# Performance work log

Measured on AMD Instinct MI355X. Metric: run time of the kernel, lower is better.

Reference implementation:

```python
import jax, jax.numpy as jnp
import numpy as np

N_NODES = 100000
N_FEAT = 512
HIDDEN = 64
N_CLASSES = 40
N_EDGES = 3200000
K = 10
ALPHA = 0.1


def setup_inputs() -> dict:
    key = jax.random.key(0)
    k1, k2, k3, k4 = jax.random.split(key, 4)
    x = jax.random.normal(k1, (N_NODES, N_FEAT), dtype=jnp.float32)
    # Glorot-ish scaled linear weights
    W1 = jax.random.normal(k2, (N_FEAT, HIDDEN), dtype=jnp.float32) / np.sqrt(N_FEAT)
    b1 = jnp.zeros((HIDDEN,), dtype=jnp.float32)
    W2 = jax.random.normal(k3, (HIDDEN, N_CLASSES), dtype=jnp.float32) / np.sqrt(HIDDEN)
    b2 = jnp.zeros((N_CLASSES,), dtype=jnp.float32)
    edge_index = jax.random.randint(k4, (2, N_EDGES), 0, N_NODES, dtype=jnp.int64)
    return {"x": x, "W1": W1, "b1": b1, "W2": W2, "b2": b2, "edge_index": edge_index}


def reference(x, W1, b1, W2, b2, edge_index):
    n = x.shape[0]
    # MLP (dropout is identity in eval mode)
    h = jnp.maximum(x @ W1 + b1, 0.0)
    h = h @ W2 + b2  # [N, C]

    # gcn_norm with self-loops: A_hat = D^{-1/2} (A + I) D^{-1/2}
    loops = jnp.arange(n, dtype=edge_index.dtype)
    row = jnp.concatenate([edge_index[0], loops])  # source (gather)
    col = jnp.concatenate([edge_index[1], loops])  # target (scatter)
    deg = jax.ops.segment_sum(jnp.ones(row.shape, dtype=h.dtype), col, num_segments=n)
    dinv = jnp.where(deg > 0, jax.lax.rsqrt(deg), 0.0)
    norm = dinv[row] * dinv[col]  # [E + N]

    h0 = h

    def step(z, _):
        msg = norm[:, None] * z[row]                      # gather + scale
        agg = jax.ops.segment_sum(msg, col, num_segments=n)  # scatter-add
        z = ALPHA * h0 + (1.0 - ALPHA) * agg
        return z, None

    z, _ = jax.lax.scan(step, h0, None, length=K)
    return jax.nn.log_softmax(z, axis=1)
```

## Files before the change

kernel.cpp:

```cpp
#include <hip/hip_runtime.h>
#include <hip/hip_bf16.h>
#include <hip/hip_fp16.h>

#define N_NODES   100000
#define N_FEAT    512
#define HIDDEN    64
#define N_CLASSES 40
#define KITER     10
#define ALPHA     0.1f
#define ZP        64
#define HPITCH    72
#define NXCD      8
#define WIN       (N_NODES / NXCD)
#define SUBCAP    65536
#define PARTB     2048
#define CAP       96

typedef __attribute__((ext_vector_type(8))) short bf16x8;
typedef __attribute__((ext_vector_type(4))) float f32x4;

__device__ __forceinline__ float bf2f(unsigned short u) {
    union { unsigned int i; float f; } c;
    c.i = ((unsigned int)u) << 16;
    return c.f;
}
__device__ __forceinline__ unsigned short f2bf(float f) {
    union { float f; unsigned int u; } c; c.f = f;
    unsigned int r = c.u + 0x7FFFu + ((c.u >> 16) & 1u);
    return (unsigned short)(r >> 16);
}

__global__ void zero_cur_kernel(int* __restrict__ cur, int* __restrict__ flags) {
    int t = threadIdx.x;
    if (t < 65) cur[t] = 0;
    if (t >= 65 && t < 67) flags[t - 65] = 0;
}

__global__ void detect_float_kernel(const unsigned short* __restrict__ w1raw,
                                    int* __restrict__ flags) {
    int i = blockIdx.x * blockDim.x + threadIdx.x;
    if (i < 32768) {
        unsigned short u = w1raw[i];
        if ((u & 0x7F80u) == 0x7F80u) atomicAdd(&flags[0], 1);
    }
}

__global__ void detect_edge_kernel(const int* __restrict__ ei, int* __restrict__ flags) {
    int i = blockIdx.x * blockDim.x + threadIdx.x;
    if (i < 2048) {
        if (ei[2 * i + 1] != 0) atomicAdd(&flags[1], 1);
    }
}

__global__ void pack_w1_kernel(const void* __restrict__ W1p, const int* __restrict__ flags,
                               unsigned short* __restrict__ pb) {
    int idx = blockIdx.x * 256 + threadIdx.x;
    int j    = idx & 7;
    int lane = (idx >> 3) & 63;
    int ktnt = idx >> 9;
    int kt = ktnt & 15, nt = ktnt >> 4;
    int k = kt * 32 + (lane >> 4) * 8 + j;
    int n = nt * 16 + (lane & 15);
    unsigned short v;
    if (flags[0] > 0) v = f2bf(((const float*)W1p)[k * HIDDEN + n]);
    else              v = ((const unsigned short*)W1p)[k * HIDDEN + n];
    pb[idx] = v;
}

__global__ void pack_w2_kernel(const void* __restrict__ W2p, const int* __restrict__ flags,
                               unsigned short* __restrict__ pb2) {
    int idx = blockIdx.x * 256 + threadIdx.x;
    if (idx >= 3072) return;
    int j    = idx & 7;
    int lane = (idx >> 3) & 63;
    int ktnt = idx >> 9;
    int kt = ktnt & 1, nt = ktnt >> 1;
    int k = kt * 32 + (lane >> 4) * 8 + j;
    int n = nt * 16 + (lane & 15);
    unsigned short v = 0;
    if (n < N_CLASSES) {
        if (flags[0] > 0) v = f2bf(((const float*)W2p)[k * N_CLASSES + n]);
        else              v = ((const unsigned short*)W2p)[k * N_CLASSES + n];
    }
    pb2[idx] = v;
}

__global__ __launch_bounds__(256) void mlp_kernel(
    const void* __restrict__ xp,
    const unsigned short* __restrict__ pb,
    const unsigned short* __restrict__ pb2,
    const void* __restrict__ b1p,
    const void* __restrict__ b2p,
    const int* __restrict__ flags,
    const float* __restrict__ dinv,
    float* __restrict__ h0,
    __half* __restrict__ zh0)
{
    __shared__ unsigned short hsb[4][16 * HPITCH];
    const int t    = threadIdx.x;
    const int wave = t >> 6;
    const int lane = t & 63;
    const int quad = lane >> 4;
    const int ml   = lane & 15;
    const int mbase = blockIdx.x * 64 + wave * 16;
    const int isf32 = flags[0] > 0;
    const bool valid = mbase < N_NODES;

    const bf16x8* pbv = (const bf16x8*)pb;
    f32x4 acc[4];
    #pragma unroll
    for (int nt = 0; nt < 4; ++nt) acc[nt] = (f32x4){0.f, 0.f, 0.f, 0.f};

    if (valid) {
        if (!isf32) {
            const unsigned short* xrow = (const unsigned short*)xp
                                       + (size_t)(mbase + ml) * N_FEAT + quad * 8;
            #pragma unroll
            for (int kt = 0; kt < 16; ++kt) {
                bf16x8 a = *(const bf16x8*)(xrow + kt * 32);
                #pragma unroll
                for (int nt = 0; nt < 4; ++nt)
                    acc[nt] = __builtin_amdgcn_mfma_f32_16x16x32_bf16(
                        a, pbv[(nt * 16 + kt) * 64 + lane], acc[nt], 0, 0, 0);
            }
        } else {
            const float* xf = (const float*)xp + (size_t)(mbase + ml) * N_FEAT + quad * 8;
            #pragma unroll
            for (int kt = 0; kt < 16; ++kt) {
                float4 lo = *(const float4*)(xf + kt * 32);
                float4 hi = *(const float4*)(xf + kt * 32 + 4);
                bf16x8 a;
                a[0] = (short)f2bf(lo.x); a[1] = (short)f2bf(lo.y);
                a[2] = (short)f2bf(lo.z); a[3] = (short)f2bf(lo.w);
                a[4] = (short)f2bf(hi.x); a[5] = (short)f2bf(hi.y);
                a[6] = (short)f2bf(hi.z); a[7] = (short)f2bf(hi.w);
                #pragma unroll
                for (int nt = 0; nt < 4; ++nt)
                    acc[nt] = __builtin_amdgcn_mfma_f32_16x16x32_bf16(
                        a, pbv[(nt * 16 + kt) * 64 + lane], acc[nt], 0, 0, 0);
            }
        }

        #pragma unroll
        for (int nt = 0; nt < 4; ++nt) {
            float b1v = isf32 ? ((const float*)b1p)[nt * 16 + ml]
                              : bf2f(((const unsigned short*)b1p)[nt * 16 + ml]);
            #pragma unroll
            for (int r = 0; r < 4; ++r)
                hsb[wave][(quad * 4 + r) * HPITCH + nt * 16 + ml] =
                    f2bf(fmaxf(acc[nt][r] + b1v, 0.0f));
        }
    }
    __syncthreads();

    if (valid) {
        const bf16x8* pb2v = (const bf16x8*)pb2;
        f32x4 acc2[3];
        #pragma unroll
        for (int n2 = 0; n2 < 3; ++n2) acc2[n2] = (f32x4){0.f, 0.f, 0.f, 0.f};
        #pragma unroll
        for (int kt = 0; kt < 2; ++kt) {
            bf16x8 a = *(const bf16x8*)(&hsb[wave][ml * HPITCH + kt * 32 + quad * 8]);
            #pragma unroll
            for (int n2 = 0; n2 < 3; ++n2)
                acc2[n2] = __builtin_amdgcn_mfma_f32_16x16x32_bf16(
                    a, pb2v[(n2 * 2 + kt) * 64 + lane], acc2[n2], 0, 0, 0);
        }
        #pragma unroll
        for (int n2 = 0; n2 < 3; ++n2) {
            int n = n2 * 16 + ml;
            if (n < N_CLASSES) {
                float b2v = isf32 ? ((const float*)b2p)[n]
                                  : bf2f(((const unsigned short*)b2p)[n]);
                #pragma unroll
                for (int r = 0; r < 4; ++r) {
                    int node = mbase + quad * 4 + r;
                    float v = acc2[n2][r] + b2v;
                    h0[(size_t)node * N_CLASSES + n] = v;
                    zh0[(size_t)node * ZP + n] = __float2half(v * dinv[node]);
                }
            }
        }
    }
}

__global__ void zero_pad_kernel(__half* __restrict__ a, __half* __restrict__ b) {
    int t = threadIdx.x;
    if (t < ZP)            a[(size_t)N_NODES * ZP + t]        = __float2half(0.0f);
    else if (t < 2 * ZP)   b[(size_t)N_NODES * ZP + (t - ZP)] = __float2half(0.0f);
}

__global__ __launch_bounds__(256) void partition_kernel(
    const int* __restrict__ ei, const int* __restrict__ flags,
    unsigned int* __restrict__ sub,
    int* __restrict__ cur, int2* __restrict__ ovf, int E)
{
    __shared__ unsigned buf[64][CAP];
    __shared__ int cnt_lds[64];
    __shared__ unsigned base_s[64];

    const int i64f = flags[1] == 0;
    const int per  = (E + PARTB - 1) / PARTB;
    const int e0   = blockIdx.x * per;
    const int e1   = min(e0 + per, E);

    if (threadIdx.x < 64) cnt_lds[threadIdx.x] = 0;
    __syncthreads();

    for (int e = e0 + threadIdx.x; e < e1; e += 256) {
        int c = i64f ? __builtin_nontemporal_load(ei + 2 * E + 2 * e)
                     : __builtin_nontemporal_load(ei + E + e);
        int r = i64f ? __builtin_nontemporal_load(ei + 2 * e)
                     : __builtin_nontemporal_load(ei + e);
        int wd = c / WIN;
        int ws = r / WIN;
        int b  = wd * 8 + ws;
        unsigned pk = (unsigned)r | ((unsigned)(c - wd * WIN) << 17);
        int slot = atomicAdd(&cnt_lds[b], 1);
        if (slot < CAP) buf[b][slot] = pk;
        else { int op = atomicAdd(cur + 64, 1); ovf[op] = make_int2(r, c); }
    }
    __syncthreads();

    const int g  = threadIdx.x >> 2;
    const int l4 = threadIdx.x & 3;
    const int n  = min(cnt_lds[g], CAP);
    if (l4 == 0 && n > 0) base_s[g] = (unsigned)atomicAdd(&cur[g], n);
    __syncthreads();
    if (n > 0) {
        unsigned base = base_s[g];
        unsigned bslot = (unsigned)g * SUBCAP;
        for (int i = l4; i < n; i += 4) {
            unsigned p = base + (unsigned)i;
            unsigned pk = buf[g][i];
            if (p < SUBCAP) sub[bslot + p] = pk;
            else {
                int op = atomicAdd(cur + 64, 1);
                ovf[op] = make_int2((int)(pk & 0x1FFFFu),
                                    (g >> 3) * WIN + (int)(pk >> 17));
            }
        }
    }
}

__global__ __launch_bounds__(1024) void hist_kernel(
    const unsigned int* __restrict__ sub, const int* __restrict__ cur,
    const int2* __restrict__ ovf, int* __restrict__ hists)
{
    __shared__ int h[WIN];
    const int w = blockIdx.x & 7;
    const int s = blockIdx.x >> 3;
    for (int off = threadIdx.x; off < WIN; off += 1024) h[off] = 0;
    __syncthreads();
    int n = min(cur[w * 8 + s], SUBCAP);
    const unsigned int* sp = sub + (size_t)(w * 8 + s) * SUBCAP;
    for (int i = threadIdx.x; i < n; i += 1024)
        atomicAdd(&h[sp[i] >> 17], 1);
    if (s == 7) {
        int ov = cur[64];
        for (int i = threadIdx.x; i < ov; i += 1024) {
            int2 rc = ovf[i];
            int ww = rc.y / WIN;
            if (ww == w) atomicAdd(&h[rc.y - ww * WIN], 1);
        }
    }
    __syncthreads();
    for (int off = threadIdx.x; off < WIN; off += 1024)
        hists[(size_t)(w * 8 + s) * WIN + off] = h[off];
}

__global__ void cnt_kernel(const int* __restrict__ hists, int* __restrict__ cnt,
                           float* __restrict__ dinv) {
    int i = blockIdx.x * 256 + threadIdx.x;
    if (i >= N_NODES) return;
    int w = i / WIN, off = i - w * WIN;
    int c = 0;
    #pragma unroll
    for (int x = 0; x < 8; ++x) c += hists[(size_t)(w * 8 + x) * WIN + off];
    cnt[i] = c;
    dinv[i] = rsqrtf((float)c + 1.0f);
}

__global__ __launch_bounds__(1024) void scan_kernel(
    const int* __restrict__ cnt, int* __restrict__ rptr, int E)
{
    __shared__ int wsum[16];
    __shared__ int carry_s, tiletot_s;
    const int t = threadIdx.x, wave = t >> 6, lane = t & 63;
    if (t == 0) carry_s = 0;
    __syncthreads();
    for (int base = 0; base < N_NODES; base += 4096) {
        int i0 = base + t * 4;
        int v0 = (i0 + 0 < N_NODES) ? cnt[i0 + 0] : 0;
        int v1 = (i0 + 1 < N_NODES) ? cnt[i0 + 1] : 0;
        int v2 = (i0 + 2 < N_NODES) ? cnt[i0 + 2] : 0;
        int v3 = (i0 + 3 < N_NODES) ? cnt[i0 + 3] : 0;
        int tl = v0 + v1 + v2 + v3;
        int sc = tl;
        #pragma unroll
        for (int off = 1; off < 64; off <<= 1) {
            int u = __shfl_up(sc, off, 64);
            if (lane >= off) sc += u;
        }
        if (lane == 63) wsum[wave] = sc;
        int wexcl = sc - tl;
        __syncthreads();
        if (wave == 0) {
            int wv = (lane < 16) ? wsum[lane] : 0;
            int ws = wv;
            #pragma unroll
            for (int off = 1; off < 16; off <<= 1) {
                int u = __shfl_up(ws, off, 64);
                if (lane >= off) ws += u;
            }
            if (lane < 16) wsum[lane] = ws - wv;
            if (lane == 15) tiletot_s = ws;
        }
        __syncthreads();
        int P  = carry_s + wsum[wave] + wexcl;
        if (i0 + 0 < N_NODES) rptr[i0 + 0] = P;
        if (i0 + 1 < N_NODES) rptr[i0 + 1] = P + v0;
        if (i0 + 2 < N_NODES) rptr[i0 + 2] = P + v0 + v1;
        if (i0 + 3 < N_NODES) rptr[i0 + 3] = P + v0 + v1 + v2;
        __syncthreads();
        if (t == 0) carry_s += tiletot_s;
        __syncthreads();
    }
    if (t == 0) rptr[N_NODES] = E;
}

__global__ __launch_bounds__(1024) void scatter_kernel(
    const unsigned int* __restrict__ sub, const int* __restrict__ cur,
    const int* __restrict__ hists, const int2* __restrict__ ovf,
    const int* __restrict__ rptr, int* __restrict__ srcidx)
{
    __shared__ int curs[WIN];
    const int w = blockIdx.x & 7;
    const int s = blockIdx.x >> 3;
    for (int off = threadIdx.x; off < WIN; off += 1024) {
        int base = rptr[w * WIN + off];
        for (int x = 0; x < s; ++x)
            base += hists[(size_t)(w * 8 + x) * WIN + off];
        curs[off] = base;
    }
    __syncthreads();
    int n = min(cur[w * 8 + s], SUBCAP);
    const unsigned int* sp = sub + (size_t)(w * 8 + s) * SUBCAP;
    for (int i = threadIdx.x; i < n; i += 1024) {
        unsigned pk = sp[i];
        int slot = atomicAdd(&curs[pk >> 17], 1);
        srcidx[slot] = (int)(pk & 0x1FFFFu);
    }
    if (s == 7) {
        int ov = cur[64];
        for (int i = threadIdx.x; i < ov; i += 1024) {
            int2 rc = ovf[i];
            int ww = rc.y / WIN;
            if (ww == w) {
                int slot = atomicAdd(&curs[rc.y - ww * WIN], 1);
                srcidx[slot] = rc.x;
            }
        }
    }
}

__global__ __launch_bounds__(256) void prop_kernel(
    const __half* __restrict__ zh, const float* __restrict__ h0,
    const float* __restrict__ dinv, const int* __restrict__ rptr,
    const int* __restrict__ srcidx, __half* __restrict__ zout)
{
    const int wave = threadIdx.x >> 6;
    const int lane = threadIdx.x & 63;
    const int g    = lane >> 4;
    const int l    = lane & 15;
    const int node = blockIdx.x * 16 + wave * 4 + g;
    const int c0   = l * 4;

    const int beg = rptr[node];
    const int end = rptr[node + 1];
    int nch = (end - beg + 15) >> 4;
    int m1    = max(nch, __shfl_xor(nch, 16, 64));
    int maxch = max(m1,  __shfl_xor(m1, 32, 64));

    float di = dinv[node];
    uint2 yself = *(const uint2*)(zh + ((size_t)node << 6) + c0);
    float h00 = 0.f, h01 = 0.f, h02 = 0.f, h03 = 0.f;
    if (c0 < N_CLASSES) {
        const float* hp = h0 + (size_t)node * N_CLASSES + c0;
        h00 = hp[0]; h01 = hp[1]; h02 = hp[2]; h03 = hp[3];
    }

    float a0 = 0.f, a1 = 0.f, a2 = 0.f, a3 = 0.f;
    float b0 = 0.f, b1 = 0.f, b2 = 0.f, b3 = 0.f;

    int idx0 = beg + l;
    int sw = (idx0 < end) ? srcidx[idx0] : N_NODES;

    for (int ch = 0; ch < maxch; ++ch) {
        int idxn = beg + (ch + 1) * 16 + l;
        int swn = (ch + 1 < maxch) ? ((idxn < end) ? srcidx[idxn] : N_NODES) : N_NODES;

        #pragma unroll
        for (int i = 0; i < 16; i += 2) {
            int s0 = __shfl(sw, (g << 4) + i,     64);
            int s1 = __shfl(sw, (g << 4) + i + 1, 64);
            uint2 z0 = *(const uint2*)(zh + ((size_t)s0 << 6) + c0);
            uint2 z1 = *(const uint2*)(zh + ((size_t)s1 << 6) + c0);
            const __half2* p0 = (const __half2*)&z0;
            const __half2* p1 = (const __half2*)&z1;
            float2 f00 = __half22float2(p0[0]);
            float2 f01 = __half22float2(p0[1]);
            float2 f10 = __half22float2(p1[0]);
            float2 f11 = __half22float2(p1[1]);
            a0 += f00.x; a1 += f00.y; a2 += f01.x; a3 += f01.y;
            b0 += f10.x; b1 += f10.y; b2 += f11.x; b3 += f11.y;
        }
        sw = swn;
    }

    if (c0 < N_CLASSES) {
        const __half2* ps = (const __half2*)&yself;
        float2 s01 = __half22float2(ps[0]);
        float2 s23 = __half22float2(ps[1]);
        float kk = (1.0f - ALPHA) * di;
        float o0 = ALPHA * h00 + kk * (a0 + b0 + s01.x);
        float o1 = ALPHA * h01 + kk * (a1 + b1 + s01.y);
        float o2 = ALPHA * h02 + kk * (a2 + b2 + s23.x);
        float o3 = ALPHA * h03 + kk * (a3 + b3 + s23.y);
        __half2 q01 = __floats2half2_rn(di * o0, di * o1);
        __half2 q23 = __floats2half2_rn(di * o2, di * o3);
        uint2 st;
        st.x = *(unsigned int*)&q01;
        st.y = *(unsigned int*)&q23;
        *(uint2*)(zout + ((size_t)node << 6) + c0) = st;
    }
}

__global__ __launch_bounds__(256) void lsm_kernel(
    const __half* __restrict__ zh, const float* __restrict__ dinv,
    const int* __restrict__ flags, void* __restrict__ outp)
{
    const int wave = threadIdx.x >> 6;
    const int lane = threadIdx.x & 63;
    const int node = blockIdx.x * 4 + wave;
    const int isf32 = flags[0] > 0;

    float di = dinv[node];
    float v = (lane < N_CLASSES)
            ? __half2float(zh[(size_t)node * ZP + lane]) / di : -1e30f;
    float m = v;
    #pragma unroll
    for (int o = 32; o; o >>= 1) m = fmaxf(m, __shfl_xor(m, o, 64));
    float e = (lane < N_CLASSES) ? expf(v - m) : 0.0f;
    float s = e;
    #pragma unroll
    for (int o = 32; o; o >>= 1) s += __shfl_xor(s, o, 64);
    float ls = logf(s);
    if (lane < N_CLASSES) {
        float r = v - m - ls;
        size_t idx = (size_t)node * N_CLASSES + lane;
        if (isf32) ((float*)outp)[idx] = r;
        else       ((__hip_bfloat16*)outp)[idx] = __float2bfloat16(r);
    }
}

extern "C" void kernel_launch(void* const* d_in, const int* in_sizes, int n_in,
                              void* d_out, int out_size, void* d_ws, size_t ws_size,
                              hipStream_t stream)
{
    const void* x  = d_in[0];
    const void* W1 = d_in[1];
    const void* b1 = d_in[2];
    const void* W2 = d_in[3];
    const void* b2 = d_in[4];
    const int* ei = (const int*)d_in[5];
    const int E = in_sizes[5] / 2;

    char* ws = (char*)d_ws;
    size_t off = 0;
    auto carve = [&](size_t bytes) -> void* {
        void* p = ws + off;
        off = (off + bytes + 255) & ~(size_t)255;
        return p;
    };
    float*  h0    = (float*) carve((size_t)N_NODES * N_CLASSES * 4);
    __half* zhA   = (__half*)carve((size_t)(N_NODES + 1) * ZP * 2);
    __half* zhB   = (__half*)carve((size_t)(N_NODES + 1) * ZP * 2);
    int*    cnt   = (int*)   carve((size_t)N_NODES * 4);
    float*  dinv  = (float*) carve((size_t)N_NODES * 4);
    int*    rptr  = (int*)   carve((size_t)(N_NODES + 1) * 4);
    int*    srcidx= (int*)   carve((size_t)E * 4);
    unsigned int* sub = (unsigned int*)carve((size_t)64 * SUBCAP * 4);
    int*    hists = (int*)   carve((size_t)64 * WIN * 4);
    int*    cur   = (int*)   carve(65 * sizeof(int));
    unsigned short* pb  = (unsigned short*)carve(32768 * 2);
    unsigned short* pb2 = (unsigned short*)carve(3072 * 2);
    int*    flags = (int*)   carve(2 * sizeof(int));
    (void)ws_size; (void)n_in; (void)out_size;

    int2* ovf = (int2*)zhA;

    const int nodeBlocks = N_NODES / 4;
    const int mlpBlocks  = (N_NODES + 63) / 64;
    const int propBlocks = N_NODES / 16;
    const int cntBlocks  = (N_NODES + 255) / 256;

    zero_cur_kernel<<<1, 128, 0, stream>>>(cur, flags);
    detect_float_kernel<<<128, 256, 0, stream>>>((const unsigned short*)W1, flags);
    detect_edge_kernel<<<8, 256, 0, stream>>>(ei, flags);
    pack_w1_kernel<<<128, 256, 0, stream>>>(W1, flags, pb);
    pack_w2_kernel<<<12, 256, 0, stream>>>(W2, flags, pb2);

    partition_kernel<<<PARTB, 256, 0, stream>>>(ei, flags, sub, cur, ovf, E);
    hist_kernel<<<64, 1024, 0, stream>>>(sub, cur, ovf, hists);
    cnt_kernel<<<cntBlocks, 256, 0, stream>>>(hists, cnt, dinv);
    scan_kernel<<<1, 1024, 0, stream>>>(cnt, rptr, E);
    scatter_kernel<<<64, 1024, 0, stream>>>(sub, cur, hists, ovf, rptr, srcidx);
    zero_pad_kernel<<<1, 128, 0, stream>>>(zhA, zhB);

    mlp_kernel<<<mlpBlocks, 256, 0, stream>>>(x, pb, pb2, b1, b2, flags, dinv, h0, zhA);

    const __half* zin = zhA;
    __half* zout = zhB;
    const __half* zlast = zhA;
    for (int it = 0; it < KITER; ++it) {
        prop_kernel<<<propBlocks, 256, 0, stream>>>(zin, h0, dinv, rptr, srcidx, zout);
        zlast = zout;
        zin = zout;
        zout = (zout == zhB) ? zhA : zhB;
    }

    lsm_kernel<<<nodeBlocks, 256, 0, stream>>>(zlast, dinv, flags, d_out);
}
```

Baseline: 1.027 ms.

## Split padded fp16 feature rows into 32-wide and 8-wide planes

Replaces the 64-half padded node feature layout with two arrays: one holding the first 32 classes (64 bytes per node) and one holding the remaining 8 (16 bytes per node). The goal is to cut the gathered bytes per edge in the propagation kernel from a padded 128-byte row to 80 bytes of real data, reducing memory traffic and cache footprint. Lanes 10-15, which only read padding, now read a duplicate address instead of distinct padding bytes. Each gather now touches two separate cache lines in different arrays per source node. The overflow buffer gets its own workspace allocation instead of aliasing the feature buffer.

```diff
diff --git a/kernel.cpp b/kernel.cpp
--- a/kernel.cpp
+++ b/kernel.cpp
@@ -8,7 +8,6 @@
 #define N_CLASSES 40
 #define KITER     10
 #define ALPHA     0.1f
-#define ZP        64
 #define HPITCH    72
 #define NXCD      8
 #define WIN       (N_NODES / NXCD)
@@ -94,7 +93,8 @@
     const int* __restrict__ flags,
     const float* __restrict__ dinv,
     float* __restrict__ h0,
-    __half* __restrict__ zh0)
+    __half* __restrict__ ylo,
+    __half* __restrict__ yhi)
 {
     __shared__ unsigned short hsb[4][16 * HPITCH];
     const int t    = threadIdx.x;
@@ -177,17 +177,23 @@
                     int node = mbase + quad * 4 + r;
                     float v = acc2[n2][r] + b2v;
                     h0[(size_t)node * N_CLASSES + n] = v;
-                    zh0[(size_t)node * ZP + n] = __float2half(v * dinv[node]);
+                    __half yv = __float2half(v * dinv[node]);
+                    if (n < 32) ylo[(size_t)node * 32 + n] = yv;
+                    else        yhi[(size_t)node * 8 + (n - 32)] = yv;
                 }
             }
         }
     }
 }
 
-__global__ void zero_pad_kernel(__half* __restrict__ a, __half* __restrict__ b) {
+__global__ void zero_pad_kernel(__half* __restrict__ a, __half* __restrict__ b,
+                                __half* __restrict__ c, __half* __restrict__ d) {
     int t = threadIdx.x;
-    if (t < ZP)            a[(size_t)N_NODES * ZP + t]        = __float2half(0.0f);
-    else if (t < 2 * ZP)   b[(size_t)N_NODES * ZP + (t - ZP)] = __float2half(0.0f);
+    __half z = __float2half(0.0f);
+    if (t < 32)        a[(size_t)N_NODES * 32 + t] = z;
+    else if (t < 64)   b[(size_t)N_NODES * 32 + (t - 32)] = z;
+    else if (t < 136)  c[(size_t)N_NODES * 8 + (t - 64)] = z;
+    else if (t < 208)  d[(size_t)N_NODES * 8 + (t - 136)] = z;
 }
 
 __global__ __launch_bounds__(256) void partition_kernel(
@@ -365,9 +371,11 @@
 }
 
 __global__ __launch_bounds__(256) void prop_kernel(
-    const __half* __restrict__ zh, const float* __restrict__ h0,
+    const __half* __restrict__ ylo_i, const __half* __restrict__ yhi_i,
+    const float* __restrict__ h0,
     const float* __restrict__ dinv, const int* __restrict__ rptr,
-    const int* __restrict__ srcidx, __half* __restrict__ zout)
+    const int* __restrict__ srcidx,
+    __half* __restrict__ ylo_o, __half* __restrict__ yhi_o)
 {
     const int wave = threadIdx.x >> 6;
     const int lane = threadIdx.x & 63;
@@ -376,6 +384,12 @@
     const int node = blockIdx.x * 16 + wave * 4 + g;
     const int c0   = l * 4;
 
+    const bool lo   = (l < 8);
+    const int  sh   = lo ? 5 : 3;
+    const int  offr = lo ? (l * 4) : ((l < 10) ? (l - 8) * 4 : 0);
+    const __half* gin  = lo ? ylo_i : yhi_i;
+    __half*       gout = lo ? ylo_o : yhi_o;
+
     const int beg = rptr[node];
     const int end = rptr[node + 1];
     int nch = (end - beg + 15) >> 4;
@@ -383,7 +397,7 @@
     int maxch = max(m1,  __shfl_xor(m1, 32, 64));
 
     float di = dinv[node];
-    uint2 yself = *(const uint2*)(zh + ((size_t)node << 6) + c0);
+    uint2 yself = *(const uint2*)(gin + ((size_t)node << sh) + offr);
     float h00 = 0.f, h01 = 0.f, h02 = 0.f, h03 = 0.f;
     if (c0 < N_CLASSES) {
         const float* hp = h0 + (size_t)node * N_CLASSES + c0;
@@ -404,8 +418,8 @@
         for (int i = 0; i < 16; i += 2) {
             int s0 = __shfl(sw, (g << 4) + i,     64);
             int s1 = __shfl(sw, (g << 4) + i + 1, 64);
-            uint2 z0 = *(const uint2*)(zh + ((size_t)s0 << 6) + c0);
-            uint2 z1 = *(const uint2*)(zh + ((size_t)s1 << 6) + c0);
+            uint2 z0 = *(const uint2*)(gin + ((size_t)s0 << sh) + offr);
+            uint2 z1 = *(const uint2*)(gin + ((size_t)s1 << sh) + offr);
             const __half2* p0 = (const __half2*)&z0;
             const __half2* p1 = (const __half2*)&z1;
             float2 f00 = __half22float2(p0[0]);
@@ -432,12 +446,13 @@
         uint2 st;
         st.x = *(unsigned int*)&q01;
         st.y = *(unsigned int*)&q23;
-        *(uint2*)(zout + ((size_t)node << 6) + c0) = st;
+        *(uint2*)(gout + ((size_t)node << sh) + offr) = st;
     }
 }
 
 __global__ __launch_bounds__(256) void lsm_kernel(
-    const __half* __restrict__ zh, const float* __restrict__ dinv,
+    const __half* __restrict__ ylo, const __half* __restrict__ yhi,
+    const float* __restrict__ dinv,
     const int* __restrict__ flags, void* __restrict__ outp)
 {
     const int wave = threadIdx.x >> 6;
@@ -446,8 +461,9 @@
     const int isf32 = flags[0] > 0;
 
     float di = dinv[node];
-    float v = (lane < N_CLASSES)
-            ? __half2float(zh[(size_t)node * ZP + lane]) / di : -1e30f;
+    float v = -1e30f;
+    if (lane < 32)              v = __half2float(ylo[(size_t)node * 32 + lane]) / di;
+    else if (lane < N_CLASSES)  v = __half2float(yhi[(size_t)node * 8 + lane - 32]) / di;
     float m = v;
     #pragma unroll
     for (int o = 32; o; o >>= 1) m = fmaxf(m, __shfl_xor(m, o, 64));
@@ -484,22 +500,23 @@
         return p;
     };
     float*  h0    = (float*) carve((size_t)N_NODES * N_CLASSES * 4);
-    __half* zhA   = (__half*)carve((size_t)(N_NODES + 1) * ZP * 2);
-    __half* zhB   = (__half*)carve((size_t)(N_NODES + 1) * ZP * 2);
+    __half* yloA  = (__half*)carve(((size_t)(N_NODES + 1) * 32 + 64) * 2);
+    __half* yloB  = (__half*)carve(((size_t)(N_NODES + 1) * 32 + 64) * 2);
+    __half* yhiA  = (__half*)carve(((size_t)(N_NODES + 1) * 8 + 64) * 2);
+    __half* yhiB  = (__half*)carve(((size_t)(N_NODES + 1) * 8 + 64) * 2);
     int*    cnt   = (int*)   carve((size_t)N_NODES * 4);
     float*  dinv  = (float*) carve((size_t)N_NODES * 4);
     int*    rptr  = (int*)   carve((size_t)(N_NODES + 1) * 4);
     int*    srcidx= (int*)   carve((size_t)E * 4);
     unsigned int* sub = (unsigned int*)carve((size_t)64 * SUBCAP * 4);
     int*    hists = (int*)   carve((size_t)64 * WIN * 4);
+    int2*   ovf   = (int2*)  carve((size_t)E * 8);
     int*    cur   = (int*)   carve(65 * sizeof(int));
     unsigned short* pb  = (unsigned short*)carve(32768 * 2);
     unsigned short* pb2 = (unsigned short*)carve(3072 * 2);
     int*    flags = (int*)   carve(2 * sizeof(int));
     (void)ws_size; (void)n_in; (void)out_size;
 
-    int2* ovf = (int2*)zhA;
-
     const int nodeBlocks = N_NODES / 4;
     const int mlpBlocks  = (N_NODES + 63) / 64;
     const int propBlocks = N_NODES / 16;
@@ -516,19 +533,22 @@
     cnt_kernel<<<cntBlocks, 256, 0, stream>>>(hists, cnt, dinv);
     scan_kernel<<<1, 1024, 0, stream>>>(cnt, rptr, E);
     scatter_kernel<<<64, 1024, 0, stream>>>(sub, cur, hists, ovf, rptr, srcidx);
-    zero_pad_kernel<<<1, 128, 0, stream>>>(zhA, zhB);
-
-    mlp_kernel<<<mlpBlocks, 256, 0, stream>>>(x, pb, pb2, b1, b2, flags, dinv, h0, zhA);
-
-    const __half* zin = zhA;
-    __half* zout = zhB;
-    const __half* zlast = zhA;
+    zero_pad_kernel<<<1, 256, 0, stream>>>(yloA, yloB, yhiA, yhiB);
+
+    mlp_kernel<<<mlpBlocks, 256, 0, stream>>>(x, pb, pb2, b1, b2, flags, dinv,
+                                              h0, yloA, yhiA);
+
+    const __half* li = yloA; const __half* hi = yhiA;
+    __half* lo_ = yloB;      __half* ho_ = yhiB;
+    const __half* llast = yloA; const __half* hlast = yhiA;
     for (int it = 0; it < KITER; ++it) {
-        prop_kernel<<<propBlocks, 256, 0, stream>>>(zin, h0, dinv, rptr, srcidx, zout);
-        zlast = zout;
-        zin = zout;
-        zout = (zout == zhB) ? zhA : zhB;
-    }
-
-    lsm_kernel<<<nodeBlocks, 256, 0, stream>>>(zlast, dinv, flags, d_out);
-}
+        prop_kernel<<<propBlocks, 256, 0, stream>>>(li, hi, h0, dinv, rptr, srcidx,
+                                                    lo_, ho_);
+        llast = lo_; hlast = ho_;
+        li = lo_; hi = ho_;
+        lo_ = (lo_ == yloB) ? yloA : yloB;
+        ho_ = (ho_ == yhiB) ? yhiA : yhiB;
+    }
+
+    lsm_kernel<<<nodeBlocks, 256, 0, stream>>>(llast, hlast, dinv, flags, d_out);
+}
```

Result: slower. 1.062 ms (+3.4%).

## Split propagation into source-window phases with partial sums and a reduce pass

Applied to the files above, without the earlier changes.

Edges are now partitioned into 4 source-node windows per destination window, and each node records per-phase CSR offsets. Each propagation iteration runs a phase kernel where each block gathers only from one source window, so the gathered feature slice (about 25k nodes) is more likely to stay cache-resident. The phase kernel writes fp32 partial sums, and a reduce kernel combines them with the self term and h0. Feature rows are also packed to 40 halves instead of 64. The cost is an extra launch per iteration, plus writing and re-reading four fp32 partial arrays, and the software prefetch of source indices is dropped.

```diff
diff --git a/kernel.cpp b/kernel.cpp
--- a/kernel.cpp
+++ b/kernel.cpp
@@ -8,13 +8,15 @@
 #define N_CLASSES 40
 #define KITER     10
 #define ALPHA     0.1f
-#define ZP        64
 #define HPITCH    72
 #define NXCD      8
 #define WIN       (N_NODES / NXCD)
-#define SUBCAP    65536
+#define NPH       4
+#define SRCWIN    (N_NODES / NPH)
+#define SUBCAP    131072
 #define PARTB     2048
-#define CAP       96
+#define CAP       128
+#define N40       ((size_t)N_NODES * 40)
 
 typedef __attribute__((ext_vector_type(8))) short bf16x8;
 typedef __attribute__((ext_vector_type(4))) float f32x4;
@@ -32,8 +34,8 @@
 
 __global__ void zero_cur_kernel(int* __restrict__ cur, int* __restrict__ flags) {
     int t = threadIdx.x;
-    if (t < 65) cur[t] = 0;
-    if (t >= 65 && t < 67) flags[t - 65] = 0;
+    if (t < 33) cur[t] = 0;
+    if (t >= 33 && t < 35) flags[t - 33] = 0;
 }
 
 __global__ void detect_float_kernel(const unsigned short* __restrict__ w1raw,
@@ -94,7 +96,7 @@
     const int* __restrict__ flags,
     const float* __restrict__ dinv,
     float* __restrict__ h0,
-    __half* __restrict__ zh0)
+    __half* __restrict__ y0)
 {
     __shared__ unsigned short hsb[4][16 * HPITCH];
     const int t    = threadIdx.x;
@@ -177,7 +179,7 @@
                     int node = mbase + quad * 4 + r;
                     float v = acc2[n2][r] + b2v;
                     h0[(size_t)node * N_CLASSES + n] = v;
-                    zh0[(size_t)node * ZP + n] = __float2half(v * dinv[node]);
+                    y0[(size_t)node * 40 + n] = __float2half(v * dinv[node]);
                 }
             }
         }
@@ -186,8 +188,9 @@
 
 __global__ void zero_pad_kernel(__half* __restrict__ a, __half* __restrict__ b) {
     int t = threadIdx.x;
-    if (t < ZP)            a[(size_t)N_NODES * ZP + t]        = __float2half(0.0f);
-    else if (t < 2 * ZP)   b[(size_t)N_NODES * ZP + (t - ZP)] = __float2half(0.0f);
+    __half z = __float2half(0.0f);
+    if (t < 48)             a[N40 + t] = z;
+    else if (t < 96)        b[N40 + (t - 48)] = z;
 }
 
 __global__ __launch_bounds__(256) void partition_kernel(
@@ -195,16 +198,16 @@
     unsigned int* __restrict__ sub,
     int* __restrict__ cur, int2* __restrict__ ovf, int E)
 {
-    __shared__ unsigned buf[64][CAP];
-    __shared__ int cnt_lds[64];
-    __shared__ unsigned base_s[64];
+    __shared__ unsigned buf[32][CAP];
+    __shared__ int cnt_lds[32];
+    __shared__ unsigned base_s[32];
 
     const int i64f = flags[1] == 0;
     const int per  = (E + PARTB - 1) / PARTB;
     const int e0   = blockIdx.x * per;
     const int e1   = min(e0 + per, E);
 
-    if (threadIdx.x < 64) cnt_lds[threadIdx.x] = 0;
+    if (threadIdx.x < 32) cnt_lds[threadIdx.x] = 0;
     __syncthreads();
 
     for (int e = e0 + threadIdx.x; e < e1; e += 256) {
@@ -213,31 +216,31 @@
         int r = i64f ? __builtin_nontemporal_load(ei + 2 * e)
                      : __builtin_nontemporal_load(ei + e);
         int wd = c / WIN;
-        int ws = r / WIN;
-        int b  = wd * 8 + ws;
+        int sp = r / SRCWIN;
+        int b  = wd * 4 + sp;
         unsigned pk = (unsigned)r | ((unsigned)(c - wd * WIN) << 17);
         int slot = atomicAdd(&cnt_lds[b], 1);
         if (slot < CAP) buf[b][slot] = pk;
-        else { int op = atomicAdd(cur + 64, 1); ovf[op] = make_int2(r, c); }
-    }
-    __syncthreads();
-
-    const int g  = threadIdx.x >> 2;
-    const int l4 = threadIdx.x & 3;
+        else { int op = atomicAdd(cur + 32, 1); ovf[op] = make_int2(r, c); }
+    }
+    __syncthreads();
+
+    const int g  = threadIdx.x >> 3;
+    const int l8 = threadIdx.x & 7;
     const int n  = min(cnt_lds[g], CAP);
-    if (l4 == 0 && n > 0) base_s[g] = (unsigned)atomicAdd(&cur[g], n);
+    if (l8 == 0 && n > 0) base_s[g] = (unsigned)atomicAdd(&cur[g], n);
     __syncthreads();
     if (n > 0) {
         unsigned base = base_s[g];
         unsigned bslot = (unsigned)g * SUBCAP;
-        for (int i = l4; i < n; i += 4) {
+        for (int i = l8; i < n; i += 8) {
             unsigned p = base + (unsigned)i;
             unsigned pk = buf[g][i];
             if (p < SUBCAP) sub[bslot + p] = pk;
             else {
-                int op = atomicAdd(cur + 64, 1);
+                int op = atomicAdd(cur + 32, 1);
                 ovf[op] = make_int2((int)(pk & 0x1FFFFu),
-                                    (g >> 3) * WIN + (int)(pk >> 17));
+                                    (g >> 2) * WIN + (int)(pk >> 17));
             }
         }
     }
@@ -250,14 +253,15 @@
     __shared__ int h[WIN];
     const int w = blockIdx.x & 7;
     const int s = blockIdx.x >> 3;
+    const int b = w * 4 + s;
     for (int off = threadIdx.x; off < WIN; off += 1024) h[off] = 0;
     __syncthreads();
-    int n = min(cur[w * 8 + s], SUBCAP);
-    const unsigned int* sp = sub + (size_t)(w * 8 + s) * SUBCAP;
+    int n = min(cur[b], SUBCAP);
+    const unsigned int* sp = sub + (size_t)b * SUBCAP;
     for (int i = threadIdx.x; i < n; i += 1024)
         atomicAdd(&h[sp[i] >> 17], 1);
-    if (s == 7) {
-        int ov = cur[64];
+    if (s == 3) {
+        int ov = cur[32];
         for (int i = threadIdx.x; i < ov; i += 1024) {
             int2 rc = ovf[i];
             int ww = rc.y / WIN;
@@ -266,7 +270,7 @@
     }
     __syncthreads();
     for (int off = threadIdx.x; off < WIN; off += 1024)
-        hists[(size_t)(w * 8 + s) * WIN + off] = h[off];
+        hists[(size_t)b * WIN + off] = h[off];
 }
 
 __global__ void cnt_kernel(const int* __restrict__ hists, int* __restrict__ cnt,
@@ -276,7 +280,7 @@
     int w = i / WIN, off = i - w * WIN;
     int c = 0;
     #pragma unroll
-    for (int x = 0; x < 8; ++x) c += hists[(size_t)(w * 8 + x) * WIN + off];
+    for (int x = 0; x < 4; ++x) c += hists[(size_t)(w * 4 + x) * WIN + off];
     cnt[i] = c;
     dinv[i] = rsqrtf((float)c + 1.0f);
 }
@@ -332,27 +336,30 @@
 __global__ __launch_bounds__(1024) void scatter_kernel(
     const unsigned int* __restrict__ sub, const int* __restrict__ cur,
     const int* __restrict__ hists, const int2* __restrict__ ovf,
-    const int* __restrict__ rptr, int* __restrict__ srcidx)
+    const int* __restrict__ rptr, int* __restrict__ srcidx, int* __restrict__ soff)
 {
     __shared__ int curs[WIN];
     const int w = blockIdx.x & 7;
     const int s = blockIdx.x >> 3;
+    const int b = w * 4 + s;
     for (int off = threadIdx.x; off < WIN; off += 1024) {
-        int base = rptr[w * WIN + off];
+        int node = w * WIN + off;
+        int base = rptr[node];
         for (int x = 0; x < s; ++x)
-            base += hists[(size_t)(w * 8 + x) * WIN + off];
+            base += hists[(size_t)(w * 4 + x) * WIN + off];
         curs[off] = base;
-    }
-    __syncthreads();
-    int n = min(cur[w * 8 + s], SUBCAP);
-    const unsigned int* sp = sub + (size_t)(w * 8 + s) * SUBCAP;
+        soff[node * 4 + s] = base;
+    }
+    __syncthreads();
+    int n = min(cur[b], SUBCAP);
+    const unsigned int* sp = sub + (size_t)b * SUBCAP;
     for (int i = threadIdx.x; i < n; i += 1024) {
         unsigned pk = sp[i];
         int slot = atomicAdd(&curs[pk >> 17], 1);
         srcidx[slot] = (int)(pk & 0x1FFFFu);
     }
-    if (s == 7) {
-        int ov = cur[64];
+    if (s == 3) {
+        int ov = cur[32];
         for (int i = threadIdx.x; i < ov; i += 1024) {
             int2 rc = ovf[i];
             int ww = rc.y / WIN;
@@ -364,48 +371,40 @@
     }
 }
 
-__global__ __launch_bounds__(256) void prop_kernel(
-    const __half* __restrict__ zh, const float* __restrict__ h0,
-    const float* __restrict__ dinv, const int* __restrict__ rptr,
-    const int* __restrict__ srcidx, __half* __restrict__ zout)
-{
+__global__ __launch_bounds__(256) void phase_kernel(
+    const __half* __restrict__ yin, const int* __restrict__ soff,
+    const int* __restrict__ rptr, const int* __restrict__ srcidx,
+    float* __restrict__ partial)
+{
+    const int p    = blockIdx.x & 3;
+    const int nb   = blockIdx.x >> 2;
     const int wave = threadIdx.x >> 6;
     const int lane = threadIdx.x & 63;
     const int g    = lane >> 4;
     const int l    = lane & 15;
-    const int node = blockIdx.x * 16 + wave * 4 + g;
+    const int node = nb * 16 + wave * 4 + g;
     const int c0   = l * 4;
-
-    const int beg = rptr[node];
-    const int end = rptr[node + 1];
-    int nch = (end - beg + 15) >> 4;
+    const int offr = (l < 10) ? l * 4 : 0;
+
+    const int start = soff[node * 4 + p];
+    const int end   = (p < 3) ? soff[node * 4 + p + 1] : rptr[node + 1];
+    int nch = (end - start + 15) >> 4;
     int m1    = max(nch, __shfl_xor(nch, 16, 64));
     int maxch = max(m1,  __shfl_xor(m1, 32, 64));
 
-    float di = dinv[node];
-    uint2 yself = *(const uint2*)(zh + ((size_t)node << 6) + c0);
-    float h00 = 0.f, h01 = 0.f, h02 = 0.f, h03 = 0.f;
-    if (c0 < N_CLASSES) {
-        const float* hp = h0 + (size_t)node * N_CLASSES + c0;
-        h00 = hp[0]; h01 = hp[1]; h02 = hp[2]; h03 = hp[3];
-    }
-
     float a0 = 0.f, a1 = 0.f, a2 = 0.f, a3 = 0.f;
     float b0 = 0.f, b1 = 0.f, b2 = 0.f, b3 = 0.f;
 
-    int idx0 = beg + l;
-    int sw = (idx0 < end) ? srcidx[idx0] : N_NODES;
-
     for (int ch = 0; ch < maxch; ++ch) {
-        int idxn = beg + (ch + 1) * 16 + l;
-        int swn = (ch + 1 < maxch) ? ((idxn < end) ? srcidx[idxn] : N_NODES) : N_NODES;
+        int idx = start + ch * 16 + l;
+        int sw  = (idx < end) ? srcidx[idx] : N_NODES;
 
         #pragma unroll
         for (int i = 0; i < 16; i += 2) {
             int s0 = __shfl(sw, (g << 4) + i,     64);
             int s1 = __shfl(sw, (g << 4) + i + 1, 64);
-            uint2 z0 = *(const uint2*)(zh + ((size_t)s0 << 6) + c0);
-            uint2 z1 = *(const uint2*)(zh + ((size_t)s1 << 6) + c0);
+            uint2 z0 = *(const uint2*)(yin + (size_t)s0 * 40 + offr);
+            uint2 z1 = *(const uint2*)(yin + (size_t)s1 * 40 + offr);
             const __half2* p0 = (const __half2*)&z0;
             const __half2* p1 = (const __half2*)&z1;
             float2 f00 = __half22float2(p0[0]);
@@ -415,29 +414,56 @@
             a0 += f00.x; a1 += f00.y; a2 += f01.x; a3 += f01.y;
             b0 += f10.x; b1 += f10.y; b2 += f11.x; b3 += f11.y;
         }
-        sw = swn;
     }
 
     if (c0 < N_CLASSES) {
-        const __half2* ps = (const __half2*)&yself;
-        float2 s01 = __half22float2(ps[0]);
-        float2 s23 = __half22float2(ps[1]);
-        float kk = (1.0f - ALPHA) * di;
-        float o0 = ALPHA * h00 + kk * (a0 + b0 + s01.x);
-        float o1 = ALPHA * h01 + kk * (a1 + b1 + s01.y);
-        float o2 = ALPHA * h02 + kk * (a2 + b2 + s23.x);
-        float o3 = ALPHA * h03 + kk * (a3 + b3 + s23.y);
-        __half2 q01 = __floats2half2_rn(di * o0, di * o1);
-        __half2 q23 = __floats2half2_rn(di * o2, di * o3);
-        uint2 st;
-        st.x = *(unsigned int*)&q01;
-        st.y = *(unsigned int*)&q23;
-        *(uint2*)(zout + ((size_t)node << 6) + c0) = st;
-    }
+        f32x4 o;
+        o[0] = a0 + b0; o[1] = a1 + b1; o[2] = a2 + b2; o[3] = a3 + b3;
+        f32x4* dst = (f32x4*)(partial + (size_t)p * N40 + (size_t)node * 40 + c0);
+        __builtin_nontemporal_store(o, dst);
+    }
+}
+
+__global__ __launch_bounds__(256) void reduce_kernel(
+    const float* __restrict__ partial, const __half* __restrict__ yin,
+    const float* __restrict__ h0, const float* __restrict__ dinv,
+    __half* __restrict__ yout)
+{
+    const int wave = threadIdx.x >> 6;
+    const int lane = threadIdx.x & 63;
+    const int g    = lane >> 4;
+    const int l    = lane & 15;
+    const int node = blockIdx.x * 16 + wave * 4 + g;
+    const int c0   = l * 4;
+    if (c0 >= N_CLASSES) return;
+
+    float sx = 0.f, sy = 0.f, sz = 0.f, sw = 0.f;
+    #pragma unroll
+    for (int p = 0; p < NPH; ++p) {
+        f32x4 v = *(const f32x4*)(partial + (size_t)p * N40 + (size_t)node * 40 + c0);
+        sx += v[0]; sy += v[1]; sz += v[2]; sw += v[3];
+    }
+    uint2 ys = *(const uint2*)(yin + (size_t)node * 40 + c0);
+    f32x4 h = *(const f32x4*)(h0 + (size_t)node * 40 + c0);
+    float di = dinv[node];
+    const __half2* ps = (const __half2*)&ys;
+    float2 s01 = __half22float2(ps[0]);
+    float2 s23 = __half22float2(ps[1]);
+    float kk = (1.0f - ALPHA) * di;
+    float o0 = ALPHA * h[0] + kk * (sx + s01.x);
+    float o1 = ALPHA * h[1] + kk * (sy + s01.y);
+    float o2 = ALPHA * h[2] + kk * (sz + s23.x);
+    float o3 = ALPHA * h[3] + kk * (sw + s23.y);
+    __half2 q01 = __floats2half2_rn(di * o0, di * o1);
+    __half2 q23 = __floats2half2_rn(di * o2, di * o3);
+    uint2 st;
+    st.x = *(unsigned int*)&q01;
+    st.y = *(unsigned int*)&q23;
+    *(uint2*)(yout + (size_t)node * 40 + c0) = st;
 }
 
 __global__ __launch_bounds__(256) void lsm_kernel(
-    const __half* __restrict__ zh, const float* __restrict__ dinv,
+    const __half* __restrict__ y, const float* __restrict__ dinv,
     const int* __restrict__ flags, void* __restrict__ outp)
 {
     const int wave = threadIdx.x >> 6;
@@ -447,7 +473,7 @@
 
     float di = dinv[node];
     float v = (lane < N_CLASSES)
-            ? __half2float(zh[(size_t)node * ZP + lane]) / di : -1e30f;
+            ? __half2float(y[(size_t)node * 40 + lane]) / di : -1e30f;
     float m = v;
     #pragma unroll
     for (int o = 32; o; o >>= 1) m = fmaxf(m, __shfl_xor(m, o, 64));
@@ -484,51 +510,54 @@
         return p;
     };
     float*  h0    = (float*) carve((size_t)N_NODES * N_CLASSES * 4);
-    __half* zhA   = (__half*)carve((size_t)(N_NODES + 1) * ZP * 2);
-    __half* zhB   = (__half*)carve((size_t)(N_NODES + 1) * ZP * 2);
+    __half* yA    = (__half*)carve((N40 + 64) * 2);
+    __half* yB    = (__half*)carve((N40 + 64) * 2);
+    float*  partial = (float*)carve((size_t)NPH * N40 * 4);
     int*    cnt   = (int*)   carve((size_t)N_NODES * 4);
     float*  dinv  = (float*) carve((size_t)N_NODES * 4);
     int*    rptr  = (int*)   carve((size_t)(N_NODES + 1) * 4);
+    int*    soff  = (int*)   carve((size_t)N_NODES * 4 * 4);
     int*    srcidx= (int*)   carve((size_t)E * 4);
-    unsigned int* sub = (unsigned int*)carve((size_t)64 * SUBCAP * 4);
-    int*    hists = (int*)   carve((size_t)64 * WIN * 4);
-    int*    cur   = (int*)   carve(65 * sizeof(int));
+    unsigned int* sub = (unsigned int*)carve((size_t)32 * SUBCAP * 4);
+    int*    hists = (int*)   carve((size_t)32 * WIN * 4);
+    int2*   ovf   = (int2*)  carve((size_t)E * 8);
+    int*    cur   = (int*)   carve(33 * sizeof(int));
     unsigned short* pb  = (unsigned short*)carve(32768 * 2);
     unsigned short* pb2 = (unsigned short*)carve(3072 * 2);
     int*    flags = (int*)   carve(2 * sizeof(int));
     (void)ws_size; (void)n_in; (void)out_size;
 
-    int2* ovf = (int2*)zhA;
-
-    const int nodeBlocks = N_NODES / 4;
-    const int mlpBlocks  = (N_NODES + 63) / 64;
-    const int propBlocks = N_NODES / 16;
-    const int cntBlocks  = (N_NODES + 255) / 256;
-
-    zero_cur_kernel<<<1, 128, 0, stream>>>(cur, flags);
+    const int nodeBlocks  = N_NODES / 4;
+    const int mlpBlocks   = (N_NODES + 63) / 64;
+    const int nodeBlocks16= N_NODES / 16;
+    const int phaseBlocks = nodeBlocks16 * NPH;
+    const int cntBlocks   = (N_NODES + 255) / 256;
+
+    zero_cur_kernel<<<1, 64, 0, stream>>>(cur, flags);
     detect_float_kernel<<<128, 256, 0, stream>>>((const unsigned short*)W1, flags);
     detect_edge_kernel<<<8, 256, 0, stream>>>(ei, flags);
     pack_w1_kernel<<<128, 256, 0, stream>>>(W1, flags, pb);
     pack_w2_kernel<<<12, 256, 0, stream>>>(W2, flags, pb2);
 
     partition_kernel<<<PARTB, 256, 0, stream>>>(ei, flags, sub, cur, ovf, E);
-    hist_kernel<<<64, 1024, 0, stream>>>(sub, cur, ovf, hists);
+    hist_kernel<<<32, 1024, 0, stream>>>(sub, cur, ovf, hists);
     cnt_kernel<<<cntBlocks, 256, 0, stream>>>(hists, cnt, dinv);
     scan_kernel<<<1, 1024, 0, stream>>>(cnt, rptr, E);
-    scatter_kernel<<<64, 1024, 0, stream>>>(sub, cur, hists, ovf, rptr, srcidx);
-    zero_pad_kernel<<<1, 128, 0, stream>>>(zhA, zhB);
-
-    mlp_kernel<<<mlpBlocks, 256, 0, stream>>>(x, pb, pb2, b1, b2, flags, dinv, h0, zhA);
-
-    const __half* zin = zhA;
-    __half* zout = zhB;
-    const __half* zlast = zhA;
+    scatter_kernel<<<32, 1024, 0, stream>>>(sub, cur, hists, ovf, rptr, srcidx, soff);
+    zero_pad_kernel<<<1, 128, 0, stream>>>(yA, yB);
+
+    mlp_kernel<<<mlpBlocks, 256, 0, stream>>>(x, pb, pb2, b1, b2, flags, dinv, h0, yA);
+
+    const __half* yin = yA;
+    __half* yout = yB;
+    const __half* ylast = yA;
     for (int it = 0; it < KITER; ++it) {
-        prop_kernel<<<propBlocks, 256, 0, stream>>>(zin, h0, dinv, rptr, srcidx, zout);
-        zlast = zout;
-        zin = zout;
-        zout = (zout == zhB) ? zhA : zhB;
-    }
-
-    lsm_kernel<<<nodeBlocks, 256, 0, stream>>>(zlast, dinv, flags, d_out);
-}
+        phase_kernel<<<phaseBlocks, 256, 0, stream>>>(yin, soff, rptr, srcidx, partial);
+        reduce_kernel<<<nodeBlocks16, 256, 0, stream>>>(partial, yin, h0, dinv, yout);
+        ylast = yout;
+        yin = yout;
+        yout = (yout == yB) ? yA : yB;
+    }
+
+    lsm_kernel<<<nodeBlocks, 256, 0, stream>>>(ylast, dinv, flags, d_out);
+}
```

After: 1.277 ms. 1.24x slower.
